# Optimization experiments

Measured on AMD Instinct MI355X. Metric: run time of the kernel, lower is better.

Reference implementation:

```python
import jax, jax.numpy as jnp
import numpy as np

N0, N1, N2 = 100000, 300000, 150000
P = 2
DIM = 64


def spmm(rows, cols, vals, dense, n_rows):
    # sparse[n_rows, n_cols] @ dense[n_cols, d] via gather + segment_sum
    return jax.ops.segment_sum(vals[:, None] * dense[cols], rows, num_segments=n_rows)


def powcat(X, p):
    # torch.cat([X**1, ..., X**p], dim=1)
    return jnp.concatenate([X ** n for n in range(1, p + 1)], axis=1)


def setup_inputs() -> dict:
    key = jax.random.key(0)
    ks = iter(jax.random.split(key, 64))

    def randn(shape, scale=1.0):
        return jax.random.normal(next(ks), shape, dtype=jnp.float32) * scale

    def sparse(nr, nc, nnz):
        r = jax.random.randint(next(ks), (nnz,), 0, nr, dtype=jnp.int32)
        c = jax.random.randint(next(ks), (nnz,), 0, nc, dtype=jnp.int32)
        v = randn((nnz,), 0.1)
        return r, c, v

    inp = {}
    inp["X0"] = randn((N0, DIM))
    inp["X1"] = randn((N1, DIM))
    inp["X2"] = randn((N2, DIM))
    for name, nr, nc, nnz in [
        ("L0", N0, N0, 1000000),
        ("L1", N1, N1, 2400000),
        ("L2", N2, N2, 1200000),
        ("D1invB1", N0, N1, 600000),
        ("D2B1TD1inv", N1, N0, 600000),
        ("B2TD2inv", N2, N1, 450000),
        ("B2D3", N1, N2, 450000),
    ]:
        r, c, v = sparse(nr, nc, nnz)
        inp[name + "_rows"], inp[name + "_cols"], inp[name + "_vals"] = r, c, v
    wscale = 1.0 / np.sqrt(DIM * P)
    for name in ["n2n", "n2e", "e2e", "e2n", "e2t", "t2e", "t2t"]:
        inp["W_" + name] = randn((DIM * P, DIM), wscale)
        inp["b_" + name] = randn((DIM,), wscale)
    return inp


def reference(X0, X1, X2,
              L0_rows, L0_cols, L0_vals,
              L1_rows, L1_cols, L1_vals,
              L2_rows, L2_cols, L2_vals,
              D1invB1_rows, D1invB1_cols, D1invB1_vals,
              D2B1TD1inv_rows, D2B1TD1inv_cols, D2B1TD1inv_vals,
              B2TD2inv_rows, B2TD2inv_cols, B2TD2inv_vals,
              B2D3_rows, B2D3_cols, B2D3_vals,
              W_n2n, b_n2n, W_n2e, b_n2e, W_e2e, b_e2e, W_e2n, b_e2n,
              W_e2t, b_e2t, W_t2e, b_t2e, W_t2t, b_t2t):
    X0c = powcat(X0, P)  # [N0, 2*d]
    X1c = powcat(X1, P)  # [N1, 2*d]
    X2c = powcat(X2, P)  # [N2, 2*d]

    n2n = spmm(L0_rows, L0_cols, L0_vals, X0c @ W_n2n + b_n2n, N0)
    n2e = spmm(D2B1TD1inv_rows, D2B1TD1inv_cols, D2B1TD1inv_vals, X0c @ W_n2e + b_n2e, N1)
    e2n = spmm(D1invB1_rows, D1invB1_cols, D1invB1_vals, X1c @ W_e2n + b_e2n, N0)
    e2e = spmm(L1_rows, L1_cols, L1_vals, X1c @ W_e2e + b_e2e, N1)
    e2t = spmm(B2TD2inv_rows, B2TD2inv_cols, B2TD2inv_vals, X1c @ W_e2t + b_e2t, N2)
    t2t = spmm(L2_rows, L2_cols, L2_vals, X2c @ W_t2t + b_t2t, N2)
    t2e = spmm(B2D3_rows, B2D3_cols, B2D3_vals, X2c @ W_t2e + b_t2e, N1)

    Y0 = 0.5 * jax.nn.relu(n2n + e2n)
    Y1 = (1.0 / 3.0) * jax.nn.relu(e2e + n2e + t2e)
    Y2 = 0.5 * jax.nn.relu(t2t + e2t)
    return (Y0, Y1, Y2)
```

## Files before the change

### kernel.cpp

```cpp
#include <hip/hip_runtime.h>
#include <hip/hip_bf16.h>


#define RPB 128
#define COL_MASK 0x7FFFFu
#define LROW_SH 19
#define DID_SH 26
#define CCOL_MASK 0x1FFFFFu
#define CLROW_SH 21
#define CBKT_SH 28
#define MAXNB 4352
#define MAXNG 544
#define GRID_BIN 256
#define SPMM_GRID 2048

#define SORT_PH     16384
#define SORT_LOG    14
#define SORT_MAXBIN 2048
#define SORT_CAP    (SORT_PH + SORT_MAXBIN)
#define MAXPH 8

typedef __attribute__((ext_vector_type(8))) short short8;
typedef __attribute__((ext_vector_type(4))) float f32x4;

__device__ __forceinline__ int   ntld_i(const int* p)   { return __builtin_nontemporal_load(p); }
__device__ __forceinline__ float ntld_f(const float* p) { return __builtin_nontemporal_load(p); }
__device__ __forceinline__ float4 ntld_f4(const float* p) {
    const unsigned long long* q = (const unsigned long long*)p;
    unsigned long long a = __builtin_nontemporal_load(q);
    unsigned long long b = __builtin_nontemporal_load(q + 1);
    float4 v;
    v.x = __uint_as_float((unsigned)a);
    v.y = __uint_as_float((unsigned)(a >> 32));
    v.z = __uint_as_float((unsigned)b);
    v.w = __uint_as_float((unsigned)(b >> 32));
    return v;
}
__device__ __forceinline__ void ntst_f4(float* p, float4 v) {
    unsigned long long a = (unsigned long long)__float_as_uint(v.x)
                         | ((unsigned long long)__float_as_uint(v.y) << 32);
    unsigned long long b = (unsigned long long)__float_as_uint(v.z)
                         | ((unsigned long long)__float_as_uint(v.w) << 32);
    unsigned long long* q = (unsigned long long*)p;
    __builtin_nontemporal_store(a, q);
    __builtin_nontemporal_store(b, q + 1);
}

__device__ __forceinline__ unsigned short f2bf(float f) {
    unsigned u = __float_as_uint(f);
    unsigned r = u + 0x7FFFu + ((u >> 16) & 1u);
    return (unsigned short)(r >> 16);
}

__device__ __forceinline__ void split8(float4 a0, float4 a1, short8& hi, short8& lo) {
    float v[8] = {a0.x, a0.y, a0.z, a0.w, a1.x, a1.y, a1.z, a1.w};
    #pragma unroll
    for (int e = 0; e < 8; ++e) {
        unsigned short h = f2bf(v[e]);
        float hf = __uint_as_float((unsigned)h << 16);
        hi[e] = (short)h;
        lo[e] = (short)f2bf(v[e] - hf);
    }
}

struct WAll { const float* w[7]; };

__global__ __launch_bounds__(256) void winit(WAll wa, unsigned short* __restrict__ frags)
{
    const int s = blockIdx.x;
    const float* __restrict__ W = wa.w[s];
    unsigned short* __restrict__ out = frags + (size_t)s * 16384;
    for (int slot = threadIdx.x; slot < 1024; slot += 256) {
        const int l  = slot & 63;
// ... 1 lines not shown
        const int kk = slot >> 8;
        const int col = nf * 16 + (l & 15);
        const int kb  = kk * 32 + 8 * (l >> 4);
        short8 vh, vl;
        #pragma unroll
        for (int e = 0; e < 8; ++e) {
            float w = W[(size_t)(kb + e) * 64 + col];
            unsigned short h = f2bf(w);
            float hf = __uint_as_float((unsigned)h << 16);
            vh[e] = (short)h;
            vl[e] = (short)f2bf(w - hf);
        }
        *(short8*)(out + ((size_t)((kk * 4 + nf) * 2 + 0) * 64 + l) * 8) = vh;
        *(short8*)(out + ((size_t)((kk * 4 + nf) * 2 + 1) * 64 + l) * 8) = vl;
    }
}

__device__ __forceinline__ void mfma_set(
    const short8 Ah[4], const short8 Al[4],
    const unsigned short* __restrict__ F, const float* __restrict__ bias,
    unsigned short* __restrict__ D, int nrows, int row0w, int l)
{
    const int lg = l >> 4, lr = l & 15;
    const short8* __restrict__ Fv = (const short8*)F;
    f32x4 acc[4];
    #pragma unroll
    for (int nf = 0; nf < 4; ++nf) {
        float b = bias[nf * 16 + lr];
        f32x4 bi = {b, b, b, b};
        acc[nf] = bi;
    }
    #pragma unroll
    for (int kk = 0; kk < 4; ++kk) {
        #pragma unroll
        for (int nf = 0; nf < 4; ++nf) {
            short8 bh = Fv[((kk * 4 + nf) * 2 + 0) * 64 + l];
            short8 bl = Fv[((kk * 4 + nf) * 2 + 1) * 64 + l];
            acc[nf] = __builtin_amdgcn_mfma_f32_16x16x32_bf16(Ah[kk], bh, acc[nf], 0, 0, 0);
            acc[nf] = __builtin_amdgcn_mfma_f32_16x16x32_bf16(Al[kk], bh, acc[nf], 0, 0, 0);
            acc[nf] = __builtin_amdgcn_mfma_f32_16x16x32_bf16(Ah[kk], bl, acc[nf], 0, 0, 0);
        }
    }
    #pragma unroll
    for (int nf = 0; nf < 4; ++nf) {
        #pragma unroll
        for (int j = 0; j < 4; ++j) {
            int row = row0w + lg * 4 + j;
            if (row < nrows)
                D[(size_t)row * 64 + nf * 16 + lr] = f2bf(acc[nf][j]);
        }
    }
}

__global__ __launch_bounds__(256) void gemm_powcat_mfma(
    const float* __restrict__ X, int nrows, int nsets,
    const unsigned short* __restrict__ F0, const float* __restrict__ b0, unsigned short* __restrict__ D0,
    const unsigned short* __restrict__ F1, const float* __restrict__ b1, unsigned short* __restrict__ D1,
    const unsigned short* __restrict__ F2, const float* __restrict__ b2, unsigned short* __restrict__ D2)
{
    __shared__ float Xs[64][68];
    const int tid = threadIdx.x;
    const int row0 = blockIdx.x * 64;

    #pragma unroll
    for (int it = 0; it < 4; ++it) {
        int idx = tid + it * 256;
        int r = idx >> 4, c4 = idx & 15;
        float4 v = make_float4(0.f, 0.f, 0.f, 0.f);
        if (row0 + r < nrows)
            v = ntld_f4(X + (size_t)(row0 + r) * 64 + c4 * 4);
        *(float4*)&Xs[r][c4 * 4] = v;
    }
    __syncthreads();

    const int w = tid >> 6, l = tid & 63;
    const int lg = l >> 4, lr = l & 15;

    short8 Ah[4], Al[4];
    #pragma unroll
    for (int kk = 0; kk < 4; ++kk) {
        const float* p = &Xs[w * 16 + lr][(kk & 1) * 32 + 8 * lg];
        float4 a0 = *(const float4*)p;
        float4 a1 = *(const float4*)(p + 4);
        if (kk >= 2) {
            a0.x *= a0.x; a0.y *= a0.y; a0.z *= a0.z; a0.w *= a0.w;
            a1.x *= a1.x; a1.y *= a1.y; a1.z *= a1.z; a1.w *= a1.w;
        }
        split8(a0, a1, Ah[kk], Al[kk]);
    }

    const int row0w = row0 + w * 16;
    mfma_set(Ah, Al, F0, b0, D0, nrows, row0w, l);
    if (nsets > 1) mfma_set(Ah, Al, F1, b1, D1, nrows, row0w, l);
    if (nsets > 2) mfma_set(Ah, Al, F2, b2, D2, nrows, row0w, l);
}

struct Bin7 {
    const int *r0, *r1, *r2, *r3, *r4, *r5, *r6;
    const int *c0, *c1, *c2, *c3, *c4, *c5, *c6;
    const float *v0, *v1, *v2, *v3, *v4, *v5, *v6;
    int p1, p2, p3, p4, p5, p6, p7;
    int t0, t1, t2, t3, t4, t5, t6;
};

struct CBase { int b[8]; };

struct Ent { int r; int tb; unsigned cw; float v; };

template<bool FULL>
__device__ __forceinline__ Ent decode(const Bin7& B, int i) {
    Ent e;
    if (i < B.p1) {
        int li = i;
        e.r = ntld_i(B.r0 + li); e.tb = B.t0;
        if (FULL) { e.cw = (unsigned)ntld_i(B.c0 + li) | (0u << DID_SH); e.v = ntld_f(B.v0 + li); }
    } else if (i < B.p2) {
        int li = i - B.p1;
        e.r = ntld_i(B.r1 + li); e.tb = B.t1;
        if (FULL) { e.cw = (unsigned)ntld_i(B.c1 + li) | (1u << DID_SH); e.v = ntld_f(B.v1 + li); }
    } else if (i < B.p3) {
        int li = i - B.p2;
        e.r = ntld_i(B.r2 + li); e.tb = B.t2;
        if (FULL) { e.cw = (unsigned)ntld_i(B.c2 + li) | (2u << DID_SH); e.v = ntld_f(B.v2 + li); }
    } else if (i < B.p4) {
        int li = i - B.p3;
        e.r = ntld_i(B.r3 + li); e.tb = B.t3;
        if (FULL) { e.cw = (unsigned)ntld_i(B.c3 + li) | (3u << DID_SH); e.v = ntld_f(B.v3 + li); }
    } else if (i < B.p5) {
        int li = i - B.p4;
        e.r = ntld_i(B.r4 + li); e.tb = B.t4;
        if (FULL) { e.cw = (unsigned)ntld_i(B.c4 + li) | (4u << DID_SH); e.v = ntld_f(B.v4 + li); }
    } else if (i < B.p6) {
        int li = i - B.p5;
        e.r = ntld_i(B.r5 + li); e.tb = B.t5;
        if (FULL) { e.cw = (unsigned)ntld_i(B.c5 + li) | (5u << DID_SH); e.v = ntld_f(B.v5 + li); }
    } else {
        int li = i - B.p6;
        e.r = ntld_i(B.r6 + li); e.tb = B.t6;
        if (FULL) { e.cw = (unsigned)ntld_i(B.c6 + li) | (6u << DID_SH); e.v = ntld_f(B.v6 + li); }
    }
    return e;
}

__global__ __launch_bounds__(1024) void bhist_grp(
    Bin7 B, int* __restrict__ gcount, int* __restrict__ ghist,
    int NG, int chunk)
{
    __shared__ int h[MAXNG];
    for (int i = threadIdx.x; i < NG; i += 1024) h[i] = 0;
    __syncthreads();
    const int s = blockIdx.x * chunk;
    int e = s + chunk;  if (e > B.p7) e = B.p7;
    for (int i = s + threadIdx.x; i < e; i += 1024) {
        Ent en = decode<false>(B, i);
        atomicAdd(&h[(en.tb + (en.r >> 7)) >> 3], 1);
    }
    __syncthreads();
    for (int i = threadIdx.x; i < NG; i += 1024) {
        int c = h[i];
        ghist[(size_t)blockIdx.x * NG + i] = c;
        if (c) atomicAdd(&gcount[i], c);
    }
}

__global__ __launch_bounds__(1024) void scatter_grpC(
    Bin7 B, CBase cb, int* __restrict__ gcur, const int* __restrict__ ghist,
    uint2* __restrict__ payA, int NG, int chunk)
{
    __shared__ int lbase[MAXNG];
    __shared__ int lcur[MAXNG];
    __shared__ int cbs[8];
    if (threadIdx.x < 8) cbs[threadIdx.x] = cb.b[threadIdx.x];
    for (int i = threadIdx.x; i < NG; i += 1024) {
        int c = ghist[(size_t)blockIdx.x * NG + i];
        lbase[i] = c ? atomicAdd(&gcur[i], c) : 0;
        lcur[i] = 0;
    }
    __syncthreads();
    const int s = blockIdx.x * chunk;
    int e = s + chunk;  if (e > B.p7) e = B.p7;
    for (int i = s + threadIdx.x; i < e; i += 1024) {
        Ent en = decode<true>(B, i);
        int b = en.tb + (en.r >> 7);
        int g = b >> 3;
        int pos = lbase[g] + atomicAdd(&lcur[g], 1);
        int did = (int)(en.cw >> DID_SH);
        unsigned colC = (en.cw & COL_MASK) + (unsigned)cbs[did];
        unsigned cwA = colC | ((unsigned)(en.r & 127) << CLROW_SH)
                     | ((unsigned)(b & 7) << CBKT_SH);
        payA[pos] = make_uint2(cwA, __float_as_uint(en.v));
    }
}

__global__ __launch_bounds__(1024) void sort_grpC(
    const uint2* __restrict__ payA, const int* __restrict__ goff,
    const int* __restrict__ gcur, int* __restrict__ rowoff,
    int* __restrict__ bend, uint2* __restrict__ payB,
    unsigned char* __restrict__ rowperm, int NBtot)
{
    __shared__ uint2 lpay[SORT_CAP];
    __shared__ int cnt[1024];
    __shared__ int off[1024];
    __shared__ unsigned char cnts8[1024];
    __shared__ int wsum[16];
    __shared__ int phstart[MAXPH + 1];
    __shared__ int s_nph, s_maxbin;

    const int g = blockIdx.x;
    const int tid = threadIdx.x;
    const int seg0 = goff[g], seg1 = gcur[g];
    const int n = seg1 - seg0;

    cnt[tid] = 0;
    if (tid == 0) s_maxbin = 0;
    __syncthreads();
    for (int i = seg0 + tid; i < seg1; i += 1024) {
        unsigned w = __builtin_nontemporal_load(&payA[i].x);
        atomicAdd(&cnt[(w >> CLROW_SH) & 1023], 1);
    }
    __syncthreads();

    const int lane = tid & 63, wv = tid >> 6;
    const int tot = cnt[tid];
    atomicMax(&s_maxbin, tot);
    cnts8[tid] = (unsigned char)(tot > 255 ? 255 : tot);
    int x = tot;
    #pragma unroll
    for (int o = 1; o < 64; o <<= 1) {
        int y = __shfl_up(x, o);
        if (lane >= o) x += y;
    }
    if (lane == 63) wsum[wv] = x;
    __syncthreads();
    if (tid < 16) {
        int ss = wsum[tid];
        #pragma unroll
        for (int o = 1; o < 16; o <<= 1) {
            int y = __shfl_up(ss, o, 16);
            if (tid >= o) ss += y;
        }
        wsum[tid] = ss;
    }
    __syncthreads();
    const int excl = (x - tot) + ((wv == 0) ? 0 : wsum[wv - 1]);
    off[tid] = excl;
    rowoff[(size_t)g * 1024 + tid] = seg0 + excl;
    {
        int b = g * 8 + (tid >> 7);
        if (b < NBtot && (tid & 127) == 127) bend[b] = seg0 + excl + tot;
    }
    __syncthreads();
    cnt[tid] = excl;
    {
        int p = excl >> SORT_LOG;
        int pprev = (tid == 0) ? -1 : (off[tid - 1] >> SORT_LOG);
        for (int q = pprev + 1; q <= p && q <= MAXPH; ++q) phstart[q] = excl;
        if (tid == 1023) s_nph = p + 1;
    }

    {
        const int myr = tid & 127, b0 = tid & ~127;
        const unsigned char myc = cnts8[tid];
        int rank = 0;
        #pragma unroll 8
        for (int r = 0; r < 128; ++r) {
            unsigned char c = cnts8[b0 + r];
            rank += (c > myc) || (c == myc && r < myr);
        }
        rowperm[(size_t)g * 1024 + b0 + rank] = (unsigned char)myr;
    }
    __syncthreads();

    const int nph = s_nph;
    if (n <= 0) return;

    if (s_maxbin <= SORT_MAXBIN && nph <= MAXPH) {
        for (int ph = 0; ph < nph; ++ph) {
            const int ps = phstart[ph];
            const int pe = (ph + 1 < nph) ? phstart[ph + 1] : n;
            for (int i = seg0 + tid; i < seg1; i += 1024) {
                unsigned long long pv = __builtin_nontemporal_load(
                    (const unsigned long long*)(payA + i));
                unsigned w = (unsigned)pv;
                int bin = (w >> CLROW_SH) & 1023;
                if ((off[bin] >> SORT_LOG) == ph) {
                    int pos = atomicAdd(&cnt[bin], 1);
                    lpay[pos - ps] = make_uint2(w, (unsigned)(pv >> 32));
                }
            }
            __syncthreads();
            for (int k = tid; k < pe - ps; k += 1024) {
                uint2 pv = lpay[k];
                unsigned long long o2 = (unsigned long long)(pv.x & CCOL_MASK)
                                      | ((unsigned long long)pv.y << 32);
                __builtin_nontemporal_store(o2,
                    (unsigned long long*)(payB + seg0 + ps + k));
            }
            __syncthreads();
        }
    } else {
        for (int i = seg0 + tid; i < seg1; i += 1024) {
            unsigned long long pv = __builtin_nontemporal_load(
                (const unsigned long long*)(payA + i));
            unsigned w = (unsigned)pv;
            int bin = (w >> CLROW_SH) & 1023;
            int pos = seg0 + atomicAdd(&cnt[bin], 1);
            payB[pos] = make_uint2(w & CCOL_MASK, (unsigned)(pv >> 32));
        }
    }
}

__global__ __launch_bounds__(1024) void scatter_grp(
    Bin7 B, int* __restrict__ gcur, const int* __restrict__ ghist,
    uint2* __restrict__ payA, int NG, int chunk)
{
    __shared__ int lbase[MAXNG];
    __shared__ int lcur[MAXNG];
    for (int i = threadIdx.x; i < NG; i += 1024) {
        int c = ghist[(size_t)blockIdx.x * NG + i];
        lbase[i] = c ? atomicAdd(&gcur[i], c) : 0;
        lcur[i] = 0;
    }
    __syncthreads();
    const int s = blockIdx.x * chunk;
    int e = s + chunk;  if (e > B.p7) e = B.p7;
    for (int i = s + threadIdx.x; i < e; i += 1024) {
        Ent en = decode<true>(B, i);
        int b = en.tb + (en.r >> 7);
        int g = b >> 3;
        int pos = lbase[g] + atomicAdd(&lcur[g], 1);
        unsigned col = en.cw & COL_MASK;
        unsigned did = en.cw >> DID_SH;
        unsigned cwA = col | ((unsigned)(en.r & 127) << LROW_SH)
                     | ((unsigned)(b & 7) << 26) | (did << 29);
        payA[pos] = make_uint2(cwA, __float_as_uint(en.v));
    }
}

__global__ __launch_bounds__(1024) void sort_grp(
    const uint2* __restrict__ payA, const int* __restrict__ goff,
    const int* __restrict__ gcur, int* __restrict__ rowoff,
    int* __restrict__ bend, uint2* __restrict__ payB,
    unsigned char* __restrict__ rowperm, int NBtot)
{
    __shared__ uint2 lpay[SORT_CAP];
    __shared__ int cnt[1024];
    __shared__ int off[1024];
    __shared__ unsigned char cnts8[1024];
    __shared__ int wsum[16];
    __shared__ int phstart[MAXPH + 1];
    __shared__ int s_nph, s_maxbin;

    const int g = blockIdx.x;
    const int tid = threadIdx.x;
    const int seg0 = goff[g], seg1 = gcur[g];
    const int n = seg1 - seg0;

    cnt[tid] = 0;
    if (tid == 0) s_maxbin = 0;
    __syncthreads();
    for (int i = seg0 + tid; i < seg1; i += 1024) {
        unsigned w = __builtin_nontemporal_load(&payA[i].x);
        atomicAdd(&cnt[(w >> 19) & 1023], 1);
    }
    __syncthreads();

    const int lane = tid & 63, wv = tid >> 6;
    const int tot = cnt[tid];
    atomicMax(&s_maxbin, tot);
    cnts8[tid] = (unsigned char)(tot > 255 ? 255 : tot);
    int x = tot;
    #pragma unroll
    for (int o = 1; o < 64; o <<= 1) {
        int y = __shfl_up(x, o);
        if (lane >= o) x += y;
    }
    if (lane == 63) wsum[wv] = x;
    __syncthreads();
    if (tid < 16) {
        int ss = wsum[tid];
        #pragma unroll
        for (int o = 1; o < 16; o <<= 1) {
            int y = __shfl_up(ss, o, 16);
            if (tid >= o) ss += y;
        }
        wsum[tid] = ss;
    }
    __syncthreads();
    const int excl = (x - tot) + ((wv == 0) ? 0 : wsum[wv - 1]);
    off[tid] = excl;
    rowoff[(size_t)g * 1024 + tid] = seg0 + excl;
    {
        int b = g * 8 + (tid >> 7);
        if (b < NBtot && (tid & 127) == 127) bend[b] = seg0 + excl + tot;
    }
    __syncthreads();
    cnt[tid] = excl;
    {
        int p = excl >> SORT_LOG;
        int pprev = (tid == 0) ? -1 : (off[tid - 1] >> SORT_LOG);
        for (int q = pprev + 1; q <= p && q <= MAXPH; ++q) phstart[q] = excl;
        if (tid == 1023) s_nph = p + 1;
    }

    {
        const int myr = tid & 127, b0 = tid & ~127;
        const unsigned char myc = cnts8[tid];
        int rank = 0;
        #pragma unroll 8
        for (int r = 0; r < 128; ++r) {
            unsigned char c = cnts8[b0 + r];
            rank += (c > myc) || (c == myc && r < myr);
        }
        rowperm[(size_t)g * 1024 + b0 + rank] = (unsigned char)myr;
    }
    __syncthreads();

    const int nph = s_nph;
    if (n <= 0) return;

    if (s_maxbin <= SORT_MAXBIN && nph <= MAXPH) {
        for (int ph = 0; ph < nph; ++ph) {
            const int ps = phstart[ph];
            const int pe = (ph + 1 < nph) ? phstart[ph + 1] : n;
            for (int i = seg0 + tid; i < seg1; i += 1024) {
                unsigned long long pv = __builtin_nontemporal_load(
                    (const unsigned long long*)(payA + i));
                unsigned w = (unsigned)pv;
                int bin = (w >> 19) & 1023;
                if ((off[bin] >> SORT_LOG) == ph) {
                    int pos = atomicAdd(&cnt[bin], 1);
                    lpay[pos - ps] = make_uint2(w, (unsigned)(pv >> 32));
                }
            }
            __syncthreads();
            for (int k = tid; k < pe - ps; k += 1024) {
                uint2 pv = lpay[k];
                unsigned cw = (pv.x & 0x03FFFFFFu) | ((pv.x >> 29) << 26);
                unsigned long long o2 = (unsigned long long)cw
                                      | ((unsigned long long)pv.y << 32);
                __builtin_nontemporal_store(o2,
                    (unsigned long long*)(payB + seg0 + ps + k));
            }
            __syncthreads();
        }
    } else {
        for (int i = seg0 + tid; i < seg1; i += 1024) {
            unsigned long long pv = __builtin_nontemporal_load(
                (const unsigned long long*)(payA + i));
            unsigned w = (unsigned)pv;
            int bin = (w >> 19) & 1023;
            int pos = seg0 + atomicAdd(&cnt[bin], 1);
            unsigned cw = (w & 0x03FFFFFFu) | ((w >> 29) << 26);
            payB[pos] = make_uint2(cw, (unsigned)(pv >> 32));
        }
    }
}

__global__ __launch_bounds__(1024) void scan_small(
    const int* __restrict__ in, int* __restrict__ boff,
    int* __restrict__ bcur, int n)
{
    __shared__ int wsum[16];
    __shared__ int carry;
    const int tid = threadIdx.x, lane = tid & 63, wv = tid >> 6;
    if (tid == 0) carry = 0;
    __syncthreads();
    for (int base = 0; base < n; base += 4096) {
        int i = base + tid * 4;
        int v0 = (i + 0 < n) ? in[i + 0] : 0;
        int v1 = (i + 1 < n) ? in[i + 1] : 0;
        int v2 = (i + 2 < n) ? in[i + 2] : 0;
        int v3 = (i + 3 < n) ? in[i + 3] : 0;
        int tsum = v0 + v1 + v2 + v3;
        int x = tsum;
        #pragma unroll
        for (int off = 1; off < 64; off <<= 1) {
            int y = __shfl_up(x, off);
            if (lane >= off) x += y;
        }
        if (lane == 63) wsum[wv] = x;
        int c0 = carry;
        __syncthreads();
        if (tid < 16) {
            int ss = wsum[tid];
            #pragma unroll
            for (int off = 1; off < 16; off <<= 1) {
                int y = __shfl_up(ss, off, 16);
                if (tid >= off) ss += y;
            }
            wsum[tid] = ss;
        }
        __syncthreads();
        int wpre = (wv == 0) ? 0 : wsum[wv - 1];
        int excl = c0 + wpre + (x - tsum);
        if (i + 0 < n) { boff[i + 0] = excl; bcur[i + 0] = excl; } excl += v0;
        if (i + 1 < n) { boff[i + 1] = excl; bcur[i + 1] = excl; } excl += v1;
        if (i + 2 < n) { boff[i + 2] = excl; bcur[i + 2] = excl; } excl += v2;
        if (i + 3 < n) { boff[i + 3] = excl; bcur[i + 3] = excl; }
        __syncthreads();
        if (tid == 0) carry = c0 + wsum[15];
        __syncthreads();
    }
}
// ... 182 lines not shown
            if (doRelu) {
                a.x = fmaxf(a.x, 0.f) * scale;
                a.y = fmaxf(a.y, 0.f) * scale;
                a.z = fmaxf(a.z, 0.f) * scale;
                a.w = fmaxf(a.w, 0.f) * scale;
            }
            ntst_f4(o, a);
        }
    }
}

extern "C" void kernel_launch(void* const* d_in, const int* in_sizes, int n_in,
                              void* d_out, int out_size, void* d_ws, size_t ws_size,
                              hipStream_t stream)
{
    const float* X0 = (const float*)d_in[0];
    const float* X1 = (const float*)d_in[1];
    const float* X2 = (const float*)d_in[2];
    const int N0 = in_sizes[0] / 64;
    const int N1 = in_sizes[1] / 64;
    const int N2 = in_sizes[2] / 64;

    auto Wp = [&](int i) { return (const float*)d_in[24 + 2 * i]; };
    auto bp = [&](int i) { return (const float*)d_in[25 + 2 * i]; };
    auto Sr = [&](int i) { return (const int*)d_in[3 + 3 * i]; };
    auto Sc = [&](int i) { return (const int*)d_in[4 + 3 * i]; };
    auto Sv = [&](int i) { return (const float*)d_in[5 + 3 * i]; };
    auto Sn = [&](int i) { return in_sizes[3 + 3 * i]; };

    const size_t offY1 = (size_t)N0 * 64;
    const size_t offY2 = (size_t)(N0 + N1) * 64;
    const float TH = 1.0f / 3.0f;

    const int NB0 = (N0 + RPB - 1) / RPB;
    const int NB1 = (N1 + RPB - 1) / RPB;
    const int NB2 = (N2 + RPB - 1) / RPB;

    float* out = (float*)d_out;
    auto align256 = [](size_t x) { return (x + 255) & ~(size_t)255; };

    const size_t FRAG_SET = 16384;
    const size_t fragB = align256(7 * FRAG_SET * sizeof(unsigned short));
    if (ws_size <= fragB) return;
    unsigned short* wfrags = (unsigned short*)d_ws;
    char* ws = (char*)d_ws + fragB;
    const size_t ws_avail = ws_size - fragB;
    auto wf = [&](int i) { return wfrags + (size_t)i * FRAG_SET; };

    WAll wa;
    for (int i = 0; i < 7; ++i) wa.w[i] = Wp(i);
    winit<<<7, 256, 0, stream>>>(wa, wfrags);

    const int NBall = NB0 + NB1 + NB2;
    const int NGall = (NBall + 7) / 8;
    const int nnzAll = Sn(0)+Sn(1)+Sn(2)+Sn(3)+Sn(4)+Sn(5)+Sn(6);
    const size_t payT1 = align256((size_t)nnzAll * sizeof(uint2));
    const size_t cntT1 = align256((size_t)(NBall + 8) * sizeof(int));
    const size_t rowT1 = align256((size_t)NGall * 1024 * sizeof(int));
    const size_t permT1 = align256((size_t)NGall * 1024);
    const size_t ghT1 = align256((size_t)GRID_BIN * NGall * sizeof(int));
    const size_t denseT1 = ((size_t)2*N0 + 3*N1 + 2*N2) * 64 * sizeof(unsigned short);
    const size_t regionT1 = denseT1 > payT1 ? denseT1 : payT1;
    const size_t needT1 = payT1 + 4 * cntT1 + rowT1 + permT1 + ghT1 + regionT1;
    const long long denseRows = (long long)2*N0 + 3LL*N1 + 2LL*N2;

    if (ws_avail >= needT1 && NBall <= MAXNB && denseRows < (1LL << 21)) {
        uint2* payB  = (uint2*)ws;
        int* goff    = (int*)(ws + payT1);
        int* gcur    = (int*)(ws + payT1 + 1 * cntT1);
        int* bend    = (int*)(ws + payT1 + 2 * cntT1);
        int* gcount  = (int*)(ws + payT1 + 3 * cntT1);
        int* rowoff  = (int*)(ws + payT1 + 4 * cntT1);
        unsigned char* rowperm = (unsigned char*)(ws + payT1 + 4 * cntT1 + rowT1);
        int* ghist   = (int*)(ws + payT1 + 4 * cntT1 + rowT1 + permT1);
        char* region = ws + payT1 + 4 * cntT1 + rowT1 + permT1 + ghT1;
        uint2* payA  = (uint2*)region;
        unsigned short* db = (unsigned short*)region;
        unsigned short* dn2n = db;
        unsigned short* de2n = dn2n + (size_t)N0 * 64;
        unsigned short* dn2e = de2n + (size_t)N1 * 64;
        unsigned short* de2e = dn2e + (size_t)N0 * 64;
        unsigned short* dt2e = de2e + (size_t)N1 * 64;
        unsigned short* de2t = dt2e + (size_t)N2 * 64;
        unsigned short* dt2t = de2t + (size_t)N1 * 64;

        Bin7 B;
        B.r0 = Sr(0); B.c0 = Sc(0); B.v0 = Sv(0);
        B.r1 = Sr(3); B.c1 = Sc(3); B.v1 = Sv(3);
        B.r2 = Sr(4); B.c2 = Sc(4); B.v2 = Sv(4);
        B.r3 = Sr(1); B.c3 = Sc(1); B.v3 = Sv(1);
        B.r4 = Sr(6); B.c4 = Sc(6); B.v4 = Sv(6);
        B.r5 = Sr(5); B.c5 = Sc(5); B.v5 = Sv(5);
        B.r6 = Sr(2); B.c6 = Sc(2); B.v6 = Sv(2);
        B.p1 = Sn(0);
        B.p2 = B.p1 + Sn(3);
        B.p3 = B.p2 + Sn(4);
        B.p4 = B.p3 + Sn(1);
        B.p5 = B.p4 + Sn(6);
        B.p6 = B.p5 + Sn(5);
        B.p7 = B.p6 + Sn(2);
        B.t0 = 0;   B.t1 = 0;
        B.t2 = NB0; B.t3 = NB0; B.t4 = NB0;
        B.t5 = NB0 + NB1; B.t6 = NB0 + NB1;

        CBase cb;
        cb.b[0] = 0;
        cb.b[1] = N0;
        cb.b[2] = N0 + N1;
        cb.b[3] = 2*N0 + N1;
        cb.b[4] = 2*N0 + 2*N1;
        cb.b[5] = 2*N0 + 2*N1 + N2;
        cb.b[6] = 2*N0 + 3*N1 + N2;
        cb.b[7] = 0;

        const int chunk = (B.p7 + GRID_BIN - 1) / GRID_BIN;
        hipMemsetAsync(gcount, 0, (size_t)NGall * sizeof(int), stream);
        bhist_grp<<<GRID_BIN, 1024, 0, stream>>>(B, gcount, ghist, NGall, chunk);
        scan_small<<<1, 1024, 0, stream>>>(gcount, goff, gcur, NGall);
        scatter_grpC<<<GRID_BIN, 1024, 0, stream>>>(B, cb, gcur, ghist, payA,
                                                    NGall, chunk);
        sort_grpC<<<NGall, 1024, 0, stream>>>(payA, goff, gcur, rowoff, bend,
                                              payB, rowperm, NBall);

        gemm_powcat_mfma<<<(N0 + 63) / 64, 256, 0, stream>>>(
            X0, N0, 2,
            wf(0), bp(0), dn2n,
            wf(1), bp(1), dn2e,
            wf(0), bp(0), dn2n);
        gemm_powcat_mfma<<<(N1 + 63) / 64, 256, 0, stream>>>(
            X1, N1, 3,
            wf(3), bp(3), de2n,
            wf(2), bp(2), de2e,
            wf(4), bp(4), de2t);
        gemm_powcat_mfma<<<(N2 + 63) / 64, 256, 0, stream>>>(
            X2, N2, 2,
            wf(5), bp(5), dt2e,
            wf(6), bp(6), dt2t,
            wf(5), bp(5), dt2e);

        const int grid = NBall < SPMM_GRID ? NBall : SPMM_GRID;
        spmm_stream_allC<<<grid, 256, 0, stream>>>(payB, rowoff, bend, rowperm,
            db, out, NB0, NB0 + NB1, NBall, N0, N1, N2);
        return;
    }

    const int NBtotA = NB0 + NB2;
    const int NBmax = NBtotA > NB1 ? NBtotA : NB1;
    const int NGmax = (NBmax + 7) / 8;
    const int nnzA = Sn(0) + Sn(3) + Sn(5) + Sn(2);
    const int nnzB = Sn(4) + Sn(6) + Sn(1);
    const int nnzMax = nnzA > nnzB ? nnzA : nnzB;

    const size_t payBsz = align256((size_t)nnzMax * sizeof(uint2));
    const size_t cntB = align256((size_t)(NBmax + 8) * sizeof(int));
    const size_t rowB = align256((size_t)NGmax * 1024 * sizeof(int));
    const size_t permB = align256((size_t)NGmax * 1024);
    const size_t ghB = align256((size_t)GRID_BIN * NGmax * sizeof(int));
    const size_t denseOff = payBsz + 4 * cntB + rowB + permB + ghB;

    uint2* bpayB = (uint2*)ws;
    int* goff    = (int*)(ws + payBsz);
    int* gcur    = (int*)(ws + payBsz + 1 * cntB);
    int* bend    = (int*)(ws + payBsz + 2 * cntB);
    int* gcount  = (int*)(ws + payBsz + 3 * cntB);
    int* rowoff  = (int*)(ws + payBsz + 4 * cntB);
    unsigned char* rowperm = (unsigned char*)(ws + payBsz + 4 * cntB + rowB);
    int* ghist   = (int*)(ws + payBsz + 4 * cntB + rowB + permB);
    unsigned short* dense = (unsigned short*)(ws + denseOff);
    uint2* payA  = (uint2*)dense;

    const size_t need_full = denseOff +
        ((size_t)N0 + N2 + N1) * 64 * sizeof(unsigned short);
    const bool fullB = (ws_avail >= need_full);

    {
        Bin7 B;
        B.r0 = Sr(0); B.c0 = Sc(0); B.v0 = Sv(0);
        B.r1 = Sr(3); B.c1 = Sc(3); B.v1 = Sv(3);
        B.r2 = Sr(5); B.c2 = Sc(5); B.v2 = Sv(5);
        B.r3 = Sr(2); B.c3 = Sc(2); B.v3 = Sv(2);
        B.r4 = B.r3; B.c4 = B.c3; B.v4 = B.v3;
        B.r5 = B.r3; B.c5 = B.c3; B.v5 = B.v3;
        B.r6 = B.r3; B.c6 = B.c3; B.v6 = B.v3;
        B.p1 = Sn(0);
        B.p2 = B.p1 + Sn(3);
        B.p3 = B.p2 + Sn(5);
        B.p4 = B.p3 + Sn(2);
        B.p5 = B.p4; B.p6 = B.p4; B.p7 = B.p4;
        B.t0 = 0; B.t1 = 0; B.t2 = NB0; B.t3 = NB0;
        B.t4 = NB0; B.t5 = NB0; B.t6 = NB0;

        const int NGA = (NBtotA + 7) / 8;
        const int chunk = (B.p7 + GRID_BIN - 1) / GRID_BIN;
        hipMemsetAsync(gcount, 0, (size_t)NGA * sizeof(int), stream);
        bhist_grp<<<GRID_BIN, 1024, 0, stream>>>(B, gcount, ghist, NGA, chunk);
        scan_small<<<1, 1024, 0, stream>>>(gcount, goff, gcur, NGA);
        scatter_grp<<<GRID_BIN, 1024, 0, stream>>>(B, gcur, ghist, payA, NGA, chunk);
        sort_grp<<<NGA, 1024, 0, stream>>>(payA, goff, gcur, rowoff, bend,
                                           bpayB, rowperm, NBtotA);

        unsigned short* dn2n = dense;
        unsigned short* de2n = dense + (size_t)N0 * 64;
        gemm_powcat_mfma<<<(N0 + 63) / 64, 256, 0, stream>>>(
            X0, N0, 1, wf(0), bp(0), dn2n,
            wf(0), bp(0), dn2n, wf(0), bp(0), dn2n);
        gemm_powcat_mfma<<<(N1 + 63) / 64, 256, 0, stream>>>(
            X1, N1, 1, wf(3), bp(3), de2n,
            wf(3), bp(3), de2n, wf(3), bp(3), de2n);
        spmm_stream7<<<NB0, 256, 0, stream>>>(bpayB, rowoff, bend, rowperm,
            dn2n, de2n, dn2n, dn2n, dn2n, dn2n, dn2n,
            out, 0, N0, 1, 1, 0.5f, 0x7F);

        unsigned short* de2t = dense;
        unsigned short* dt2t = dense + (size_t)N1 * 64;
        gemm_powcat_mfma<<<(N1 + 63) / 64, 256, 0, stream>>>(
            X1, N1, 1, wf(4), bp(4), de2t,
            wf(4), bp(4), de2t, wf(4), bp(4), de2t);
        gemm_powcat_mfma<<<(N2 + 63) / 64, 256, 0, stream>>>(
            X2, N2, 1, wf(6), bp(6), dt2t,
            wf(6), bp(6), dt2t, wf(6), bp(6), dt2t);
        spmm_stream7<<<NB2, 256, 0, stream>>>(bpayB, rowoff, bend, rowperm,
            de2t, de2t, de2t, dt2t, de2t, de2t, de2t,
            out + offY2, NB0, N2, 1, 1, 0.5f, 0x7F);
    }

    {
        Bin7 B;
        B.r0 = Sr(4); B.c0 = Sc(4); B.v0 = Sv(4);
        B.r1 = Sr(6); B.c1 = Sc(6); B.v1 = Sv(6);
        B.r2 = Sr(1); B.c2 = Sc(1); B.v2 = Sv(1);
        B.r3 = B.r2; B.c3 = B.c2; B.v3 = B.v2;
        B.r4 = B.r2; B.c4 = B.c2; B.v4 = B.v2;
        B.r5 = B.r2; B.c5 = B.c2; B.v5 = B.v2;
        B.r6 = B.r2; B.c6 = B.c2; B.v6 = B.v2;
        B.p1 = Sn(4);
        B.p2 = B.p1 + Sn(6);
        B.p3 = B.p2 + Sn(1);
        B.p4 = B.p3; B.p5 = B.p3; B.p6 = B.p3; B.p7 = B.p3;
        B.t0 = 0; B.t1 = 0; B.t2 = 0; B.t3 = 0; B.t4 = 0; B.t5 = 0; B.t6 = 0;

        const int NGB = (NB1 + 7) / 8;
        const int chunk = (B.p7 + GRID_BIN - 1) / GRID_BIN;
        hipMemsetAsync(gcount, 0, (size_t)NGB * sizeof(int), stream);
        bhist_grp<<<GRID_BIN, 1024, 0, stream>>>(B, gcount, ghist, NGB, chunk);
        scan_small<<<1, 1024, 0, stream>>>(gcount, goff, gcur, NGB);
        scatter_grp<<<GRID_BIN, 1024, 0, stream>>>(B, gcur, ghist, payA, NGB, chunk);
        sort_grp<<<NGB, 1024, 0, stream>>>(payA, goff, gcur, rowoff, bend,
                                           bpayB, rowperm, NB1);

        if (fullB) {
            unsigned short* dn2e = dense;
            unsigned short* dt2e = dense + (size_t)N0 * 64;
            unsigned short* de2e = dense + ((size_t)N0 + N2) * 64;
            gemm_powcat_mfma<<<(N0 + 63) / 64, 256, 0, stream>>>(
                X0, N0, 1, wf(1), bp(1), dn2e,
                wf(1), bp(1), dn2e, wf(1), bp(1), dn2e);
            gemm_powcat_mfma<<<(N2 + 63) / 64, 256, 0, stream>>>(
                X2, N2, 1, wf(5), bp(5), dt2e,
                wf(5), bp(5), dt2e, wf(5), bp(5), dt2e);
            gemm_powcat_mfma<<<(N1 + 63) / 64, 256, 0, stream>>>(
                X1, N1, 1, wf(2), bp(2), de2e,
                wf(2), bp(2), de2e, wf(2), bp(2), de2e);
            spmm_stream7<<<NB1, 256, 0, stream>>>(bpayB, rowoff, bend, rowperm,
                dn2e, dt2e, de2e, dn2e, dn2e, dn2e, dn2e,
                out + offY1, 0, N1, 1, 1, TH, 0x7F);
        } else {
            unsigned short* dn2e = dense;
            unsigned short* dt2e = dense + (size_t)N0 * 64;
            gemm_powcat_mfma<<<(N0 + 63) / 64, 256, 0, stream>>>(
                X0, N0, 1, wf(1), bp(1), dn2e,
                wf(1), bp(1), dn2e, wf(1), bp(1), dn2e);
            gemm_powcat_mfma<<<(N2 + 63) / 64, 256, 0, stream>>>(
                X2, N2, 1, wf(5), bp(5), dt2e,
                wf(5), bp(5), dt2e, wf(5), bp(5), dt2e);
            spmm_stream7<<<NB1, 256, 0, stream>>>(bpayB, rowoff, bend, rowperm,
                dn2e, dt2e, dn2e, dn2e, dn2e, dn2e, dn2e,
                out + offY1, 0, N1, 1, 0, 0.f, 0x3);
            unsigned short* de2e = dense;
            gemm_powcat_mfma<<<(N1 + 63) / 64, 256, 0, stream>>>(
                X1, N1, 1, wf(2), bp(2), de2e,
                wf(2), bp(2), de2e, wf(2), bp(2), de2e);
            spmm_stream7<<<NB1, 256, 0, stream>>>(bpayB, rowoff, bend, rowperm,
                de2e, de2e, de2e, de2e, de2e, de2e, de2e,
                out + offY1, 0, N1, 0, 1, TH, 0x4);
        }
    }
}
```

Baseline: 490.5 us.

## Halve sort groups to 4 buckets and add LDS-resident single-pass sort path

Each sort group now covers 4 buckets (512 local rows) instead of 8. That makes most groups small enough to keep the whole segment in LDS, where a counting sort over a 16-bit index array replaces the multi-phase re-reads of the payload from global memory. The three per-set GEMM launches are also merged into one launch that dispatches blocks by range. The cost is twice as many sort blocks and higher LDS usage per block, which may lower occupancy.

```diff
diff --git a/kernel.cpp b/kernel.cpp
--- a/kernel.cpp
+++ b/kernel.cpp
@@ -10,15 +10,18 @@
 #define CLROW_SH 21
 #define CBKT_SH 28
 #define MAXNB 4352
-#define MAXNG 544
+#define GBK 4
+#define GSH 2
+#define NBIN 512
+#define MAXNG 1088
 #define GRID_BIN 256
 #define SPMM_GRID 2048
 
-#define SORT_PH     16384
-#define SORT_LOG    14
-#define SORT_MAXBIN 2048
-#define SORT_CAP    (SORT_PH + SORT_MAXBIN)
-#define MAXPH 8
+#define CAPS        15744
+#define SORT_PH     8192
+#define SORT_LOG    13
+#define SORT_MAXBIN 7552
+#define MAXPH 16
 
 typedef __attribute__((ext_vector_type(8))) short short8;
 typedef __attribute__((ext_vector_type(4))) float f32x4;
@@ -126,16 +129,14 @@
     }
 }
 
-__global__ __launch_bounds__(256) void gemm_powcat_mfma(
-    const float* __restrict__ X, int nrows, int nsets,
-    const unsigned short* __restrict__ F0, const float* __restrict__ b0, unsigned short* __restrict__ D0,
-    const unsigned short* __restrict__ F1, const float* __restrict__ b1, unsigned short* __restrict__ D1,
-    const unsigned short* __restrict__ F2, const float* __restrict__ b2, unsigned short* __restrict__ D2)
-{
-    __shared__ float Xs[64][68];
+__device__ __forceinline__ void gemm_body(
+    const float* __restrict__ X, int nrows, int nsets, int row0,
+    const unsigned short* F0, const float* b0, unsigned short* D0,
+    const unsigned short* F1, const float* b1, unsigned short* D1,
+    const unsigned short* F2, const float* b2, unsigned short* D2,
+    float Xs[64][68])
+{
     const int tid = threadIdx.x;
-    const int row0 = blockIdx.x * 64;
-
     #pragma unroll
     for (int it = 0; it < 4; ++it) {
         int idx = tid + it * 256;
@@ -167,6 +168,39 @@
     mfma_set(Ah, Al, F0, b0, D0, nrows, row0w, l);
     if (nsets > 1) mfma_set(Ah, Al, F1, b1, D1, nrows, row0w, l);
     if (nsets > 2) mfma_set(Ah, Al, F2, b2, D2, nrows, row0w, l);
+}
+
+__global__ __launch_bounds__(256) void gemm_powcat_mfma(
+    const float* __restrict__ X, int nrows, int nsets,
+    const unsigned short* __restrict__ F0, const float* __restrict__ b0, unsigned short* __restrict__ D0,
+    const unsigned short* __restrict__ F1, const float* __restrict__ b1, unsigned short* __restrict__ D1,
+    const unsigned short* __restrict__ F2, const float* __restrict__ b2, unsigned short* __restrict__ D2)
+{
+    __shared__ float Xs[64][68];
+    gemm_body(X, nrows, nsets, blockIdx.x * 64,
+              F0, b0, D0, F1, b1, D1, F2, b2, D2, Xs);
+}
+
+struct GemmJob {
+    const float* X[3];
+    const unsigned short* F[9];
+    const float* bias[9];
+    unsigned short* D[9];
+    int nrows[3];
+    int nsets[3];
+    int blk0[4];
+};
+
+__global__ __launch_bounds__(256) void gemm_powcat_all(GemmJob J)
+{
+    __shared__ float Xs[64][68];
+    const int bid = blockIdx.x;
+    const int s = (bid >= J.blk0[1] ? 1 : 0) + (bid >= J.blk0[2] ? 1 : 0);
+    const int row0 = (bid - J.blk0[s]) * 64;
+    gemm_body(J.X[s], J.nrows[s], J.nsets[s], row0,
+              J.F[s*3+0], J.bias[s*3+0], J.D[s*3+0],
+              J.F[s*3+1], J.bias[s*3+1], J.D[s*3+1],
+              J.F[s*3+2], J.bias[s*3+2], J.D[s*3+2], Xs);
 }
 
 struct Bin7 {
@@ -227,7 +261,7 @@
     int e = s + chunk;  if (e > B.p7) e = B.p7;
     for (int i = s + threadIdx.x; i < e; i += 1024) {
         Ent en = decode<false>(B, i);
-        atomicAdd(&h[(en.tb + (en.r >> 7)) >> 3], 1);
+        atomicAdd(&h[(en.tb + (en.r >> 7)) >> GSH], 1);
     }
     __syncthreads();
     for (int i = threadIdx.x; i < NG; i += 1024) {
@@ -256,12 +290,12 @@
     for (int i = s + threadIdx.x; i < e; i += 1024) {
         Ent en = decode<true>(B, i);
         int b = en.tb + (en.r >> 7);
-        int g = b >> 3;
+        int g = b >> GSH;
         int pos = lbase[g] + atomicAdd(&lcur[g], 1);
         int did = (int)(en.cw >> DID_SH);
         unsigned colC = (en.cw & COL_MASK) + (unsigned)cbs[did];
         unsigned cwA = colC | ((unsigned)(en.r & 127) << CLROW_SH)
-                     | ((unsigned)(b & 7) << CBKT_SH);
+                     | ((unsigned)(b & (GBK - 1)) << CBKT_SH);
         payA[pos] = make_uint2(cwA, __float_as_uint(en.v));
     }
 }
@@ -272,11 +306,12 @@
     int* __restrict__ bend, uint2* __restrict__ payB,
     unsigned char* __restrict__ rowperm, int NBtot)
 {
-    __shared__ uint2 lpay[SORT_CAP];
-    __shared__ int cnt[1024];
-    __shared__ int off[1024];
-    __shared__ unsigned char cnts8[1024];
-    __shared__ int wsum[16];
+    __shared__ uint2 lpay[CAPS];
+    __shared__ unsigned short sidx[CAPS];
+    __shared__ int cnt[NBIN];
+    __shared__ int off[NBIN];
+    __shared__ unsigned char cnts8[NBIN];
+    __shared__ int wsum[8];
     __shared__ int phstart[MAXPH + 1];
     __shared__ int s_nph, s_maxbin;
 
@@ -284,55 +319,55 @@
     const int tid = threadIdx.x;
     const int seg0 = goff[g], seg1 = gcur[g];
     const int n = seg1 - seg0;
-
-    cnt[tid] = 0;
+    const bool fast = (n <= CAPS);
+
+    if (tid < NBIN) cnt[tid] = 0;
     if (tid == 0) s_maxbin = 0;
     __syncthreads();
     for (int i = seg0 + tid; i < seg1; i += 1024) {
-        unsigned w = __builtin_nontemporal_load(&payA[i].x);
-        atomicAdd(&cnt[(w >> CLROW_SH) & 1023], 1);
+        unsigned long long pv = __builtin_nontemporal_load(
+            (const unsigned long long*)(payA + i));
+        unsigned w = (unsigned)pv;
+        if (fast) lpay[i - seg0] = make_uint2(w, (unsigned)(pv >> 32));
+        atomicAdd(&cnt[(w >> CLROW_SH) & (NBIN - 1)], 1);
     }
     __syncthreads();
 
     const int lane = tid & 63, wv = tid >> 6;
-    const int tot = cnt[tid];
-    atomicMax(&s_maxbin, tot);
-    cnts8[tid] = (unsigned char)(tot > 255 ? 255 : tot);
+    const int tot = (tid < NBIN) ? cnt[tid] : 0;
+    if (tid < NBIN) {
+        atomicMax(&s_maxbin, tot);
+        cnts8[tid] = (unsigned char)(tot > 255 ? 255 : tot);
+    }
     int x = tot;
     #pragma unroll
     for (int o = 1; o < 64; o <<= 1) {
         int y = __shfl_up(x, o);
         if (lane >= o) x += y;
     }
-    if (lane == 63) wsum[wv] = x;
-    __syncthreads();
-    if (tid < 16) {
-        int ss = wsum[tid];
+    if (lane == 63 && wv < 8) wsum[wv] = x;
+    __syncthreads();
+    if (tid == 0) {
+        int acc = 0;
         #pragma unroll
-        for (int o = 1; o < 16; o <<= 1) {
-            int y = __shfl_up(ss, o, 16);
-            if (tid >= o) ss += y;
-        }
-        wsum[tid] = ss;
-    }
-    __syncthreads();
-    const int excl = (x - tot) + ((wv == 0) ? 0 : wsum[wv - 1]);
-    off[tid] = excl;
-    rowoff[(size_t)g * 1024 + tid] = seg0 + excl;
-    {
-        int b = g * 8 + (tid >> 7);
+        for (int j = 0; j < 8; ++j) { int t = wsum[j]; wsum[j] = acc; acc += t; }
+    }
+    __syncthreads();
+    int excl = 0;
+    if (tid < NBIN) {
+        excl = (x - tot) + wsum[wv];
+        off[tid] = excl;
+        rowoff[(size_t)g * NBIN + tid] = seg0 + excl;
+        int b = g * GBK + (tid >> 7);
         if (b < NBtot && (tid & 127) == 127) bend[b] = seg0 + excl + tot;
     }
     __syncthreads();
-    cnt[tid] = excl;
-    {
+    if (tid < NBIN) {
+        cnt[tid] = excl;
         int p = excl >> SORT_LOG;
         int pprev = (tid == 0) ? -1 : (off[tid - 1] >> SORT_LOG);
         for (int q = pprev + 1; q <= p && q <= MAXPH; ++q) phstart[q] = excl;
-        if (tid == 1023) s_nph = p + 1;
-    }
-
-    {
+        if (tid == NBIN - 1) s_nph = p + 1;
         const int myr = tid & 127, b0 = tid & ~127;
         const unsigned char myc = cnts8[tid];
         int rank = 0;
@@ -341,14 +376,28 @@
             unsigned char c = cnts8[b0 + r];
             rank += (c > myc) || (c == myc && r < myr);
         }
-        rowperm[(size_t)g * 1024 + b0 + rank] = (unsigned char)myr;
-    }
-    __syncthreads();
-
-    const int nph = s_nph;
+        rowperm[(size_t)g * NBIN + b0 + rank] = (unsigned char)myr;
+    }
+    __syncthreads();
+
     if (n <= 0) return;
 
-    if (s_maxbin <= SORT_MAXBIN && nph <= MAXPH) {
+    if (fast) {
+        for (int i = tid; i < n; i += 1024) {
+            int bin = (int)(lpay[i].x >> CLROW_SH) & (NBIN - 1);
+            int pos = atomicAdd(&cnt[bin], 1);
+            sidx[pos] = (unsigned short)i;
+        }
+        __syncthreads();
+        for (int k = tid; k < n; k += 1024) {
+            uint2 pv = lpay[sidx[k]];
+            unsigned long long o2 = (unsigned long long)(pv.x & CCOL_MASK)
+                                  | ((unsigned long long)pv.y << 32);
+            __builtin_nontemporal_store(o2,
+                (unsigned long long*)(payB + seg0 + k));
+        }
+    } else if (s_maxbin <= SORT_MAXBIN && s_nph <= MAXPH) {
+        const int nph = s_nph;
         for (int ph = 0; ph < nph; ++ph) {
             const int ps = phstart[ph];
             const int pe = (ph + 1 < nph) ? phstart[ph + 1] : n;
@@ -356,7 +405,7 @@
                 unsigned long long pv = __builtin_nontemporal_load(
                     (const unsigned long long*)(payA + i));
                 unsigned w = (unsigned)pv;
-                int bin = (w >> CLROW_SH) & 1023;
+                int bin = (w >> CLROW_SH) & (NBIN - 1);
                 if ((off[bin] >> SORT_LOG) == ph) {
                     int pos = atomicAdd(&cnt[bin], 1);
                     lpay[pos - ps] = make_uint2(w, (unsigned)(pv >> 32));
@@ -377,7 +426,7 @@
             unsigned long long pv = __builtin_nontemporal_load(
                 (const unsigned long long*)(payA + i));
             unsigned w = (unsigned)pv;
-            int bin = (w >> CLROW_SH) & 1023;
+            int bin = (w >> CLROW_SH) & (NBIN - 1);
             int pos = seg0 + atomicAdd(&cnt[bin], 1);
             payB[pos] = make_uint2(w & CCOL_MASK, (unsigned)(pv >> 32));
         }
@@ -401,12 +450,12 @@
     for (int i = s + threadIdx.x; i < e; i += 1024) {
         Ent en = decode<true>(B, i);
         int b = en.tb + (en.r >> 7);
-        int g = b >> 3;
+        int g = b >> GSH;
         int pos = lbase[g] + atomicAdd(&lcur[g], 1);
         unsigned col = en.cw & COL_MASK;
         unsigned did = en.cw >> DID_SH;
         unsigned cwA = col | ((unsigned)(en.r & 127) << LROW_SH)
-                     | ((unsigned)(b & 7) << 26) | (did << 29);
+                     | ((unsigned)(b & (GBK - 1)) << 26) | (did << 29);
         payA[pos] = make_uint2(cwA, __float_as_uint(en.v));
     }
 }
@@ -417,11 +466,12 @@
     int* __restrict__ bend, uint2* __restrict__ payB,
     unsigned char* __restrict__ rowperm, int NBtot)
 {
-    __shared__ uint2 lpay[SORT_CAP];
-    __shared__ int cnt[1024];
-    __shared__ int off[1024];
-    __shared__ unsigned char cnts8[1024];
-    __shared__ int wsum[16];
+    __shared__ uint2 lpay[CAPS];
+    __shared__ unsigned short sidx[CAPS];
+    __shared__ int cnt[NBIN];
+    __shared__ int off[NBIN];
+    __shared__ unsigned char cnts8[NBIN];
+    __shared__ int wsum[8];
     __shared__ int phstart[MAXPH + 1];
     __shared__ int s_nph, s_maxbin;
 
@@ -429,55 +479,55 @@
     const int tid = threadIdx.x;
     const int seg0 = goff[g], seg1 = gcur[g];
     const int n = seg1 - seg0;
-
-    cnt[tid] = 0;
+    const bool fast = (n <= CAPS);
+
+    if (tid < NBIN) cnt[tid] = 0;
     if (tid == 0) s_maxbin = 0;
     __syncthreads();
     for (int i = seg0 + tid; i < seg1; i += 1024) {
-        unsigned w = __builtin_nontemporal_load(&payA[i].x);
-        atomicAdd(&cnt[(w >> 19) & 1023], 1);
+        unsigned long long pv = __builtin_nontemporal_load(
+            (const unsigned long long*)(payA + i));
+        unsigned w = (unsigned)pv;
+        if (fast) lpay[i - seg0] = make_uint2(w, (unsigned)(pv >> 32));
+        atomicAdd(&cnt[(w >> 19) & (NBIN - 1)], 1);
     }
     __syncthreads();
 
     const int lane = tid & 63, wv = tid >> 6;
-    const int tot = cnt[tid];
-    atomicMax(&s_maxbin, tot);
-    cnts8[tid] = (unsigned char)(tot > 255 ? 255 : tot);
+    const int tot = (tid < NBIN) ? cnt[tid] : 0;
+    if (tid < NBIN) {
+        atomicMax(&s_maxbin, tot);
+        cnts8[tid] = (unsigned char)(tot > 255 ? 255 : tot);
+    }
     int x = tot;
     #pragma unroll
     for (int o = 1; o < 64; o <<= 1) {
         int y = __shfl_up(x, o);
         if (lane >= o) x += y;
     }
-    if (lane == 63) wsum[wv] = x;
-    __syncthreads();
-    if (tid < 16) {
-        int ss = wsum[tid];
+    if (lane == 63 && wv < 8) wsum[wv] = x;
+    __syncthreads();
+    if (tid == 0) {
+        int acc = 0;
         #pragma unroll
-        for (int o = 1; o < 16; o <<= 1) {
-            int y = __shfl_up(ss, o, 16);
-            if (tid >= o) ss += y;
-        }
-        wsum[tid] = ss;
-    }
-    __syncthreads();
-    const int excl = (x - tot) + ((wv == 0) ? 0 : wsum[wv - 1]);
-    off[tid] = excl;
-    rowoff[(size_t)g * 1024 + tid] = seg0 + excl;
-    {
-        int b = g * 8 + (tid >> 7);
+        for (int j = 0; j < 8; ++j) { int t = wsum[j]; wsum[j] = acc; acc += t; }
+    }
+    __syncthreads();
+    int excl = 0;
+    if (tid < NBIN) {
+        excl = (x - tot) + wsum[wv];
+        off[tid] = excl;
+        rowoff[(size_t)g * NBIN + tid] = seg0 + excl;
+        int b = g * GBK + (tid >> 7);
         if (b < NBtot && (tid & 127) == 127) bend[b] = seg0 + excl + tot;
     }
     __syncthreads();
-    cnt[tid] = excl;
-    {
+    if (tid < NBIN) {
+        cnt[tid] = excl;
         int p = excl >> SORT_LOG;
         int pprev = (tid == 0) ? -1 : (off[tid - 1] >> SORT_LOG);
         for (int q = pprev + 1; q <= p && q <= MAXPH; ++q) phstart[q] = excl;
-        if (tid == 1023) s_nph = p + 1;
-    }
-
-    {
+        if (tid == NBIN - 1) s_nph = p + 1;
         const int myr = tid & 127, b0 = tid & ~127;
         const unsigned char myc = cnts8[tid];
         int rank = 0;
@@ -486,14 +536,29 @@
             unsigned char c = cnts8[b0 + r];
             rank += (c > myc) || (c == myc && r < myr);
         }
-        rowperm[(size_t)g * 1024 + b0 + rank] = (unsigned char)myr;
-    }
-    __syncthreads();
-
-    const int nph = s_nph;
+        rowperm[(size_t)g * NBIN + b0 + rank] = (unsigned char)myr;
+    }
+    __syncthreads();
+
     if (n <= 0) return;
 
-    if (s_maxbin <= SORT_MAXBIN && nph <= MAXPH) {
+    if (fast) {
+        for (int i = tid; i < n; i += 1024) {
+            int bin = (int)(lpay[i].x >> 19) & (NBIN - 1);
+            int pos = atomicAdd(&cnt[bin], 1);
+            sidx[pos] = (unsigned short)i;
+        }
+        __syncthreads();
+        for (int k = tid; k < n; k += 1024) {
+            uint2 pv = lpay[sidx[k]];
+            unsigned cw = (pv.x & 0x03FFFFFFu) | ((pv.x >> 29) << 26);
+            unsigned long long o2 = (unsigned long long)cw
+                                  | ((unsigned long long)pv.y << 32);
+            __builtin_nontemporal_store(o2,
+                (unsigned long long*)(payB + seg0 + k));
+        }
+    } else if (s_maxbin <= SORT_MAXBIN && s_nph <= MAXPH) {
+        const int nph = s_nph;
         for (int ph = 0; ph < nph; ++ph) {
             const int ps = phstart[ph];
             const int pe = (ph + 1 < nph) ? phstart[ph + 1] : n;
@@ -501,7 +566,7 @@
                 unsigned long long pv = __builtin_nontemporal_load(
                     (const unsigned long long*)(payA + i));
                 unsigned w = (unsigned)pv;
-                int bin = (w >> 19) & 1023;
+                int bin = (w >> 19) & (NBIN - 1);
                 if ((off[bin] >> SORT_LOG) == ph) {
                     int pos = atomicAdd(&cnt[bin], 1);
                     lpay[pos - ps] = make_uint2(w, (unsigned)(pv >> 32));
@@ -523,7 +588,7 @@
             unsigned long long pv = __builtin_nontemporal_load(
                 (const unsigned long long*)(payA + i));
             unsigned w = (unsigned)pv;
-            int bin = (w >> 19) & 1023;
+            int bin = (w >> 19) & (NBIN - 1);
             int pos = seg0 + atomicAdd(&cnt[bin], 1);
             unsigned cw = (w & 0x03FFFFFFu) | ((w >> 29) << 26);
             payB[pos] = make_uint2(cw, (unsigned)(pv >> 32));
@@ -812,12 +877,12 @@
     winit<<<7, 256, 0, stream>>>(wa, wfrags);
 
     const int NBall = NB0 + NB1 + NB2;
-    const int NGall = (NBall + 7) / 8;
+    const int NGall = (NBall + GBK - 1) / GBK;
     const int nnzAll = Sn(0)+Sn(1)+Sn(2)+Sn(3)+Sn(4)+Sn(5)+Sn(6);
     const size_t payT1 = align256((size_t)nnzAll * sizeof(uint2));
     const size_t cntT1 = align256((size_t)(NBall + 8) * sizeof(int));
-    const size_t rowT1 = align256((size_t)NGall * 1024 * sizeof(int));
-    const size_t permT1 = align256((size_t)NGall * 1024);
+    const size_t rowT1 = align256((size_t)NGall * NBIN * sizeof(int));
+    const size_t permT1 = align256((size_t)NGall * NBIN);
     const size_t ghT1 = align256((size_t)GRID_BIN * NGall * sizeof(int));
     const size_t denseT1 = ((size_t)2*N0 + 3*N1 + 2*N2) * 64 * sizeof(unsigned short);
     const size_t regionT1 = denseT1 > payT1 ? denseT1 : payT1;
@@ -882,21 +947,23 @@
         sort_grpC<<<NGall, 1024, 0, stream>>>(payA, goff, gcur, rowoff, bend,
                                               payB, rowperm, NBall);
 
-        gemm_powcat_mfma<<<(N0 + 63) / 64, 256, 0, stream>>>(
-            X0, N0, 2,
-            wf(0), bp(0), dn2n,
-            wf(1), bp(1), dn2e,
-            wf(0), bp(0), dn2n);
-        gemm_powcat_mfma<<<(N1 + 63) / 64, 256, 0, stream>>>(
-            X1, N1, 3,
-            wf(3), bp(3), de2n,
-            wf(2), bp(2), de2e,
-            wf(4), bp(4), de2t);
-        gemm_powcat_mfma<<<(N2 + 63) / 64, 256, 0, stream>>>(
-            X2, N2, 2,
-            wf(5), bp(5), dt2e,
-            wf(6), bp(6), dt2t,
-            wf(5), bp(5), dt2e);
+        GemmJob J;
+        J.X[0] = X0; J.X[1] = X1; J.X[2] = X2;
+        J.nrows[0] = N0; J.nrows[1] = N1; J.nrows[2] = N2;
+        J.nsets[0] = 2;  J.nsets[1] = 3;  J.nsets[2] = 2;
+        J.F[0] = wf(0); J.bias[0] = bp(0); J.D[0] = dn2n;
+        J.F[1] = wf(1); J.bias[1] = bp(1); J.D[1] = dn2e;
+        J.F[2] = wf(0); J.bias[2] = bp(0); J.D[2] = dn2n;
+        J.F[3] = wf(3); J.bias[3] = bp(3); J.D[3] = de2n;
+        J.F[4] = wf(2); J.bias[4] = bp(2); J.D[4] = de2e;
+        J.F[5] = wf(4); J.bias[5] = bp(4); J.D[5] = de2t;
+        J.F[6] = wf(5); J.bias[6] = bp(5); J.D[6] = dt2e;
+        J.F[7] = wf(6); J.bias[7] = bp(6); J.D[7] = dt2t;
+        J.F[8] = wf(5); J.bias[8] = bp(5); J.D[8] = dt2e;
+        const int gb0 = (N0 + 63) / 64, gb1 = (N1 + 63) / 64, gb2 = (N2 + 63) / 64;
+        J.blk0[0] = 0; J.blk0[1] = gb0; J.blk0[2] = gb0 + gb1;
+        J.blk0[3] = gb0 + gb1 + gb2;
+        gemm_powcat_all<<<J.blk0[3], 256, 0, stream>>>(J);
 
         const int grid = NBall < SPMM_GRID ? NBall : SPMM_GRID;
         spmm_stream_allC<<<grid, 256, 0, stream>>>(payB, rowoff, bend, rowperm,
@@ -906,15 +973,15 @@
 
     const int NBtotA = NB0 + NB2;
     const int NBmax = NBtotA > NB1 ? NBtotA : NB1;
-    const int NGmax = (NBmax + 7) / 8;
+    const int NGmax = (NBmax + GBK - 1) / GBK;
     const int nnzA = Sn(0) + Sn(3) + Sn(5) + Sn(2);
     const int nnzB = Sn(4) + Sn(6) + Sn(1);
     const int nnzMax = nnzA > nnzB ? nnzA : nnzB;
 
     const size_t payBsz = align256((size_t)nnzMax * sizeof(uint2));
     const size_t cntB = align256((size_t)(NBmax + 8) * sizeof(int));
-    const size_t rowB = align256((size_t)NGmax * 1024 * sizeof(int));
-    const size_t permB = align256((size_t)NGmax * 1024);
+    const size_t rowB = align256((size_t)NGmax * NBIN * sizeof(int));
+    const size_t permB = align256((size_t)NGmax * NBIN);
     const size_t ghB = align256((size_t)GRID_BIN * NGmax * sizeof(int));
     const size_t denseOff = payBsz + 4 * cntB + rowB + permB + ghB;
 
@@ -950,7 +1017,7 @@
         B.t0 = 0; B.t1 = 0; B.t2 = NB0; B.t3 = NB0;
         B.t4 = NB0; B.t5 = NB0; B.t6 = NB0;
 
-        const int NGA = (NBtotA + 7) / 8;
+        const int NGA = (NBtotA + GBK - 1) / GBK;
         const int chunk = (B.p7 + GRID_BIN - 1) / GRID_BIN;
         hipMemsetAsync(gcount, 0, (size_t)NGA * sizeof(int), stream);
         bhist_grp<<<GRID_BIN, 1024, 0, stream>>>(B, gcount, ghist, NGA, chunk);
@@ -999,7 +1066,7 @@
         B.p4 = B.p3; B.p5 = B.p3; B.p6 = B.p3; B.p7 = B.p3;
         B.t0 = 0; B.t1 = 0; B.t2 = 0; B.t3 = 0; B.t4 = 0; B.t5 = 0; B.t6 = 0;
 
-        const int NGB = (NB1 + 7) / 8;
+        const int NGB = (NB1 + GBK - 1) / GBK;
         const int chunk = (B.p7 + GRID_BIN - 1) / GRID_BIN;
         hipMemsetAsync(gcount, 0, (size_t)NGB * sizeof(int), stream);
         bhist_grp<<<GRID_BIN, 1024, 0, stream>>>(B, gcount, ghist, NGB, chunk);
```

Result: no change. 491.7 us (+0.2%).
